# Optimization experiments

Hardware: AMD Instinct MI355X
Metric: run time of the kernel (lower is better)

## Reference

```python
import jax, jax.numpy as jnp
import numpy as np

N, E, D, ED, L = 40000, 640000, 128, 16, 3  # nodes, edges, emb_dim, edge_dim, num_layer
BN_EPS = 1e-5


def setup_inputs() -> dict:
    key = jax.random.key(0)
    ks = jax.random.split(key, 20)
    s = 0.05
    inp = {
        "x": jax.random.normal(ks[0], (N, D), jnp.float32),
        "edge_attr": jax.random.normal(ks[1], (E, ED), jnp.float32),
        # node encoder Linear(input_dim, emb_dim)
        "node_W": jax.random.normal(ks[2], (D, D), jnp.float32) * s,
        "node_b": jnp.zeros((D,), jnp.float32),
        # per-layer params (leading dim L)
        "edge_W": jax.random.normal(ks[3], (L, ED, D), jnp.float32) * s,
        "edge_b": jnp.zeros((L, D), jnp.float32),
        "attn_W": jax.random.normal(ks[4], (L, 2 * D, 1), jnp.float32) * s,
        "attn_b": jnp.zeros((L, 1), jnp.float32),
        "eps": jnp.zeros((L,), jnp.float32),
        "W1": jax.random.normal(ks[5], (L, D, 2 * D), jnp.float32) * s,
        "b1": jnp.zeros((L, 2 * D), jnp.float32),
        "bn1_g": jnp.ones((L, 2 * D), jnp.float32),
        "bn1_b": jnp.zeros((L, 2 * D), jnp.float32),
        "W2": jax.random.normal(ks[6], (L, 2 * D, D), jnp.float32) * s,
        "b2": jnp.zeros((L, D), jnp.float32),
        "bn_g": jnp.ones((L, D), jnp.float32),
        "bn_b": jnp.zeros((L, D), jnp.float32),
        "edge_index": jax.random.randint(ks[7], (2, E), 0, N, jnp.int32),
    }
    return inp


def _bn_eval(h, g, b):
    # BatchNorm1d in eval with running_mean=0, running_var=1
    return g * h * (1.0 / np.sqrt(1.0 + BN_EPS)) + b


def reference(x, edge_attr, node_W, node_b, edge_W, edge_b, attn_W, attn_b,
              eps, W1, b1, bn1_g, bn1_b, W2, b2, bn_g, bn_b, edge_index):
    src, dst = edge_index[0], edge_index[1]
    h = x @ node_W + node_b  # node_encoder, [N, D]
    for l in range(L):
        e = edge_attr @ edge_W[l] + edge_b[l]       # [E, D] edge embedding
        xj = h[src]                                  # [E, D] source gather
        xi = h[dst]                                  # [E, D] target gather
        a = jax.nn.sigmoid(jnp.concatenate([xi, xj], axis=-1) @ attn_W[l] + attn_b[l])  # [E,1]
        msg = jax.nn.relu(xj * a + e)                # fused per-edge message
        agg = jax.ops.segment_sum(msg, dst, num_segments=N)  # scatter-add aggregate
        z = (1.0 + eps[l]) * h + agg
        # GIN mlp: Linear -> BN(eval) -> ReLU -> Linear
        z = _bn_eval(z @ W1[l] + b1[l], bn1_g[l], bn1_b[l])
        z = jax.nn.relu(z)
        z = z @ W2[l] + b2[l]
        # outer BatchNorm(eval); dropout = identity in eval; JK='last', no residual
        z = _bn_eval(z, bn_g[l], bn_b[l])
        if l < L - 1:
            z = jax.nn.relu(z)
        h = z
    return h
```

## Files before the change

### kernel.cpp

```cpp
#include <hip/hip_runtime.h>
#include <math.h>

#define NN 40000
#define EE 640000
#define DD 128
#define EDD 16
#define LL 3
#define TEB 64

__device__ __constant__ float kBnInv = 0.9999950000374997f;

typedef __bf16 bf16x8 __attribute__((ext_vector_type(8)));
typedef float  f32x16 __attribute__((ext_vector_type(16)));
typedef float  f32x4  __attribute__((ext_vector_type(4)));
typedef float  f32x2  __attribute__((ext_vector_type(2)));

__device__ __forceinline__ unsigned pack_bf2(float a, float b) {
    unsigned ua = __float_as_uint(a), ub = __float_as_uint(b);
    ua = (ua + 0x7fffu + ((ua >> 16) & 1u)) >> 16;
    ub = (ub + 0x7fffu + ((ub >> 16) & 1u)) & 0xffff0000u;
    return ua | ub;
}
__device__ __forceinline__ unsigned short bf16r(float x) {
    unsigned u = __float_as_uint(x);
    u = (u + 0x7fffu + ((u >> 16) & 1u)) >> 16;
    return (unsigned short)u;
}

__global__ __launch_bounds__(256) void node_enc_kernel(
    const float* __restrict__ x, const float* __restrict__ W,
    const float* __restrict__ b,
    const float* __restrict__ aW, const float* __restrict__ eps_p,
    float* __restrict__ h, unsigned* __restrict__ hb,
    float* __restrict__ pi, float* __restrict__ pj, float* __restrict__ z)
{
    __shared__ float xs[32][DD];
    const int t = threadIdx.x;
    const long rowbase = (long)blockIdx.x * 32;

    const float4* x4 = (const float4*)(x + rowbase * DD);
    float4* xs4 = (float4*)&xs[0][0];
#pragma unroll
    for (int i = 0; i < 4; i++) xs4[t + i * 256] = x4[t + i * 256];
    __syncthreads();

    const int c  = (t & 31) * 4;
    const int r0 = (t >> 5) * 4;

    float acc[4][4] = {};
    for (int k4 = 0; k4 < DD; k4 += 4) {
        float4 xr[4];
#pragma unroll
        for (int i = 0; i < 4; i++) xr[i] = *(const float4*)&xs[r0 + i][k4];
#pragma unroll
        for (int kk = 0; kk < 4; kk++) {
            const float4 w = *(const float4*)(W + (k4 + kk) * DD + c);
#pragma unroll
            for (int i = 0; i < 4; i++) {
                const float xv = ((const float*)&xr[i])[kk];
                acc[i][0] = fmaf(xv, w.x, acc[i][0]);
                acc[i][1] = fmaf(xv, w.y, acc[i][1]);
                acc[i][2] = fmaf(xv, w.z, acc[i][2]);
                acc[i][3] = fmaf(xv, w.w, acc[i][3]);
            }
        }
    }
    const float4 bv  = *(const float4*)(b + c);
    const float4 awi = *(const float4*)(aW + c);
    const float4 awj = *(const float4*)(aW + DD + c);
    const float ep = 1.0f + eps_p[0];

    float pa[4], pb[4];
#pragma unroll
    for (int i = 0; i < 4; i++) {
        const long row = rowbase + r0 + i;
        float4 ov = { acc[i][0] + bv.x, acc[i][1] + bv.y,
                      acc[i][2] + bv.z, acc[i][3] + bv.w };
        *(float4*)(h + row * DD + c) = ov;
        uint2 pv = { pack_bf2(ov.x, ov.y), pack_bf2(ov.z, ov.w) };
        *(uint2*)(hb + row * 64 + (c >> 1)) = pv;
        float4 zv = { ep * ov.x, ep * ov.y, ep * ov.z, ep * ov.w };
        *(float4*)(z + row * DD + c) = zv;
        pa[i] = ov.x * awi.x + ov.y * awi.y + ov.z * awi.z + ov.w * awi.w;
        pb[i] = ov.x * awj.x + ov.y * awj.y + ov.z * awj.z + ov.w * awj.w;
    }
#pragma unroll
    for (int off = 1; off < 32; off <<= 1) {
#pragma unroll
        for (int i = 0; i < 4; i++) {
            pa[i] += __shfl_xor(pa[i], off, 64);
            pb[i] += __shfl_xor(pb[i], off, 64);
        }
    }
    if ((t & 31) == 0) {
#pragma unroll
        for (int i = 0; i < 4; i++) {
            pi[rowbase + r0 + i] = pa[i];
            pj[rowbase + r0 + i] = pb[i];
        }
    }
}

__global__ __launch_bounds__(256) void wcast_kernel(
    const float* __restrict__ W1, const float* __restrict__ W2,
    const float* __restrict__ eW,
    unsigned short* __restrict__ w1t, unsigned short* __restrict__ w2t,
    unsigned short* __restrict__ ewt)
{
    const int idx = blockIdx.x * 256 + threadIdx.x;
    const int l = idx >> 15, r = idx & 32767;
    {   const int n = r >> 7, k = r & 127;
        w1t[idx] = bf16r(W1[(l << 15) + (k << 8) + n]);
    }
    {   const int n = r >> 8, k = r & 255;
        w2t[idx] = bf16r(W2[(l << 15) + (k << 7) + n]);
    }
    if (idx < LL * 2048) {
        const int le = idx >> 11, re = idx & 2047;
        const int n = re >> 4, k = re & 15;
        ewt[idx] = bf16r(eW[(le << 11) + (k << 7) + n]);
    }
}

__global__ __launch_bounds__(256) void hist_kernel(
    const int* __restrict__ edge_index, int* __restrict__ counts)
{
    const int i = blockIdx.x * 256 + threadIdx.x;
    atomicAdd(&counts[edge_index[EE + i]], 1);
}

__global__ __launch_bounds__(256) void scan1_kernel(
    const int* __restrict__ counts, int* __restrict__ scanned,
    int* __restrict__ partials)
{
    __shared__ int sdata[256];
    const int t = threadIdx.x;
    const int base = blockIdx.x * 1024 + t * 4;
    int v[4]; int sum = 0;
#pragma unroll
    for (int i = 0; i < 4; i++) {
        const int idx = base + i;
        v[i] = (idx < NN) ? counts[idx] : 0;
        sum += v[i];
    }
    sdata[t] = sum;
    __syncthreads();
    for (int off = 1; off < 256; off <<= 1) {
        int x = (t >= off) ? sdata[t - off] : 0;
        __syncthreads();
        sdata[t] += x;
        __syncthreads();
    }
    int run = sdata[t] - sum;
#pragma unroll
    for (int i = 0; i < 4; i++) {
        const int idx = base + i;
        if (idx < NN) scanned[idx] = run;
        run += v[i];
    }
    if (t == 255) partials[blockIdx.x] = sdata[255];
}

__global__ void scan2_kernel(int* __restrict__ partials)
{
    if (threadIdx.x == 0) {
        int run = 0;
        for (int i = 0; i < 40; i++) { int v = partials[i]; partials[i] = run; run += v; }
    }
}

__global__ __launch_bounds__(256) void scan3_kernel(
    const int* __restrict__ scanned, const int* __restrict__ partials,
    int* __restrict__ offsets, int* __restrict__ cursor)
{
    const int idx = blockIdx.x * 256 + threadIdx.x;
    if (idx < NN) {
        const int off = scanned[idx] + partials[idx >> 10];
        offsets[idx] = off;
        cursor[idx]  = off;
    }
}

__global__ __launch_bounds__(256) void scatter_kernel(
    const int* __restrict__ edge_index, const float* __restrict__ edge_attr,
    int* __restrict__ cursor,
    int* __restrict__ srcs_p, int* __restrict__ dstd_p,
    unsigned* __restrict__ ea_b)
{
    const int i = blockIdx.x * 256 + threadIdx.x;
    const int src = edge_index[i];
    const int dst = edge_index[EE + i];
    const int pos = atomicAdd(&cursor[dst], 1);
    srcs_p[pos] = src << 6;
    dstd_p[pos] = dst << 7;

    const float4* sp = (const float4*)(edge_attr + (long)i * EDD);
    const float4 s0 = sp[0], s1 = sp[1], s2 = sp[2], s3 = sp[3];
    uint4 o0 = { pack_bf2(s0.x, s0.y), pack_bf2(s0.z, s0.w),
                 pack_bf2(s1.x, s1.y), pack_bf2(s1.z, s1.w) };
    uint4 o1 = { pack_bf2(s2.x, s2.y), pack_bf2(s2.z, s2.w),
                 pack_bf2(s3.x, s3.y), pack_bf2(s3.z, s3.w) };
    *(uint4*)(ea_b + (long)pos * 8)     = o0;
    *(uint4*)(ea_b + (long)pos * 8 + 4) = o1;
}

__global__ __launch_bounds__(256) void edge_msg_kernel(
    const unsigned* __restrict__ hb, const unsigned* __restrict__ ea_b,
    const float* __restrict__ pi, const float* __restrict__ pj,
    const int* __restrict__ srcs_p, const int* __restrict__ dstd_p,
    const float* __restrict__ ab_p,
    const unsigned short* __restrict__ eWt, const float* __restrict__ eb,
    float* __restrict__ z)
{
    __shared__ float sh_e[TEB * DD];
    __shared__ int   sh_src[TEB];
    __shared__ int   sh_dst[TEB];
    __shared__ float sh_a[TEB];

    const int t = threadIdx.x;
    const int wid = t >> 6, lane = t & 63;
    const long e0 = (long)blockIdx.x * TEB;

    if (t < TEB) {
        const int ss = srcs_p[e0 + t];
        const int dd = dstd_p[e0 + t];
        sh_src[t] = ss;
        sh_dst[t] = dd;
        const float s = pi[dd >> 7] + pj[ss >> 6] + ab_p[0];
        sh_a[t] = 1.0f / (1.0f + expf(-s));
    }

    const int l31 = lane & 31, half = lane >> 5;
    const int mt = wid & 1, nt0 = wid >> 1;
    const bf16x8 afr  = *(const bf16x8*)(ea_b + (e0 + mt * 32 + l31) * 8 + half * 4);
    const bf16x8 bfr0 = *(const bf16x8*)(eWt + (nt0 * 32 + l31) * 16 + half * 8);
    const bf16x8 bfr1 = *(const bf16x8*)(eWt + ((nt0 + 2) * 32 + l31) * 16 + half * 8);

    __syncthreads();

    const int base = wid * 16;
    unsigned u[16];
#pragma unroll
    for (int j = 0; j < 16; j++)
        u[j] = hb[sh_src[base + j] + lane];

    {
        f32x16 a0 = {0.0f,0.0f,0.0f,0.0f, 0.0f,0.0f,0.0f,0.0f,
                     0.0f,0.0f,0.0f,0.0f, 0.0f,0.0f,0.0f,0.0f};
        f32x16 a1 = a0;
        a0 = __builtin_amdgcn_mfma_f32_32x32x16_bf16(afr, bfr0, a0, 0, 0, 0);
        a1 = __builtin_amdgcn_mfma_f32_32x32x16_bf16(afr, bfr1, a1, 0, 0, 0);
        const float eb0 = eb[nt0 * 32 + l31];
        const float eb1 = eb[(nt0 + 2) * 32 + l31];
        const int rb = mt * 32 + 4 * half;
#pragma unroll
        for (int r = 0; r < 16; r++) {
            const int row = rb + (r & 3) + 8 * (r >> 2);
            sh_e[row * DD + nt0 * 32 + l31]       = a0[r] + eb0;
            sh_e[row * DD + (nt0 + 2) * 32 + l31] = a1[r] + eb1;
        }
    }
    __syncthreads();

    const int c0 = lane * 2;
    const f32x2 zero2 = { 0.0f, 0.0f };
    f32x2 acc = zero2;
    int cur = sh_dst[base];

#pragma unroll
    for (int j = 0; j < 16; j++) {
        const int dd = sh_dst[base + j];
        if (dd != cur) {
            atomicAdd(&z[cur + c0],     acc[0]);
            atomicAdd(&z[cur + c0 + 1], acc[1]);
            acc = zero2; cur = dd;
        }
        const float a = sh_a[base + j];
        const f32x2 ev = *(const f32x2*)&sh_e[(base + j) * DD + c0];
        const f32x2 xj = { __uint_as_float(u[j] << 16),
                           __uint_as_float(u[j] & 0xffff0000u) };
        const f32x2 av = { a, a };
        f32x2 m = __builtin_elementwise_fma(xj, av, ev);
        m = __builtin_elementwise_max(m, zero2);
        acc += m;
    }
    atomicAdd(&z[cur + c0],     acc[0]);
    atomicAdd(&z[cur + c0 + 1], acc[1]);
}

__global__ __launch_bounds__(256) void mlp_mfma_kernel(
    const float* __restrict__ zin,
    const unsigned short* __restrict__ w1t, const unsigned short* __restrict__ w2t,
    const float* __restrict__ b1, const float* __restrict__ g1, const float* __restrict__ bb1,
    const float* __restrict__ b2, const float* __restrict__ g2, const float* __restrict__ bb2,
    const float* __restrict__ aWn, const float* __restrict__ epsn_p,
    float* __restrict__ out, unsigned* __restrict__ hb,
    float* __restrict__ pi, float* __restrict__ pj, float* __restrict__ z,
    const int do_relu)
{
    __shared__ __align__(16) unsigned short zsb[64][136];
    __shared__ __align__(16) unsigned short usb[64][264];
    __shared__ float sh_pi[64], sh_pj[64];
    const int t = threadIdx.x;
    const int wid = t >> 6, lane = t & 63;
    const long rowbase = (long)blockIdx.x * 64;

    if (t < 64) { sh_pi[t] = 0.0f; sh_pj[t] = 0.0f; }

    {
        const float4* z4 = (const float4*)(zin + rowbase * DD);
#pragma unroll
        for (int i = 0; i < 8; i++) {
            const int idx = t + i * 256;
            const float4 v = z4[idx];
            const int row = idx >> 5;
            const int c4  = (idx & 31) * 4;
            uint2 pv = { pack_bf2(v.x, v.y), pack_bf2(v.z, v.w) };
            *(uint2*)&zsb[row][c4] = pv;
        }
    }
    __syncthreads();

    const int mrow  = lane & 15;
    const int quad  = lane >> 4;
    const f32x4 vzero = {0.0f, 0.0f, 0.0f, 0.0f};

    {
        const int nt0 = wid * 4;
        bf16x8 bf[4][4];
#pragma unroll
        for (int j = 0; j < 4; j++) {
            const unsigned short* wp = w1t + ((nt0 + j) * 16 + mrow) * 128 + quad * 8;
#pragma unroll
            for (int ks = 0; ks < 4; ks++)
                bf[j][ks] = *(const bf16x8*)(wp + ks * 32);
        }
        float gg[4], bi[4], bt[4];
#pragma unroll
        for (int j = 0; j < 4; j++) {
            const int c = (nt0 + j) * 16 + mrow;
            gg[j] = g1[c]; bi[j] = b1[c]; bt[j] = bb1[c];
        }
#pragma unroll
        for (int rt = 0; rt < 4; rt++) {
            bf16x8 af[4];
#pragma unroll
            for (int ks = 0; ks < 4; ks++)
                af[ks] = *(const bf16x8*)&zsb[rt * 16 + mrow][ks * 32 + quad * 8];
            f32x4 acc[4];
#pragma unroll
            for (int j = 0; j < 4; j++) acc[j] = vzero;
#pragma unroll
            for (int j = 0; j < 4; j++)
#pragma unroll
                for (int ks = 0; ks < 4; ks++)
                    acc[j] = __builtin_amdgcn_mfma_f32_16x16x32_bf16(af[ks], bf[j][ks], acc[j], 0, 0, 0);
#pragma unroll
            for (int j = 0; j < 4; j++) {
                const int c = (nt0 + j) * 16 + mrow;
#pragma unroll
                for (int r = 0; r < 4; r++) {
                    const int row = rt * 16 + quad * 4 + r;
                    const float u = fmaxf(fmaf(gg[j] * (acc[j][r] + bi[j]), kBnInv, bt[j]), 0.0f);
                    const float up = __shfl_xor(u, 1, 64);
                    if ((mrow & 1) == 0)
                        *(unsigned*)&usb[row][c] = pack_bf2(u, up);
                }
            }
        }
    }
    __syncthreads();

    {
        const int nt0 = wid * 2;
        bf16x8 bf[2][8];
#pragma unroll
        for (int j = 0; j < 2; j++) {
            const unsigned short* wp = w2t + ((nt0 + j) * 16 + mrow) * 256 + quad * 8;
#pragma unroll
            for (int ks = 0; ks < 8; ks++)
                bf[j][ks] = *(const bf16x8*)(wp + ks * 32);
        }
        float gg[2], bi[2], bt[2], awi[2], awj[2];
#pragma unroll
        for (int j = 0; j < 2; j++) {
            const int c = (nt0 + j) * 16 + mrow;
            gg[j] = g2[c]; bi[j] = b2[c]; bt[j] = bb2[c];
            awi[j] = aWn[c]; awj[j] = aWn[DD + c];
        }
        const float epn = do_relu ? (1.0f + epsn_p[0]) : 0.0f;

#pragma unroll
        for (int rt = 0; rt < 4; rt++) {
            bf16x8 af[8];
#pragma unroll
            for (int ks = 0; ks < 8; ks++)
                af[ks] = *(const bf16x8*)&usb[rt * 16 + mrow][ks * 32 + quad * 8];
            f32x4 acc[2];
            acc[0] = vzero; acc[1] = vzero;
#pragma unroll
            for (int j = 0; j < 2; j++)
#pragma unroll
                for (int ks = 0; ks < 8; ks++)
                    acc[j] = __builtin_amdgcn_mfma_f32_16x16x32_bf16(af[ks], bf[j][ks], acc[j], 0, 0, 0);

            float si[4] = {0, 0, 0, 0}, sj[4] = {0, 0, 0, 0};
#pragma unroll
            for (int j = 0; j < 2; j++) {
                const int c = (nt0 + j) * 16 + mrow;
#pragma unroll
                for (int r = 0; r < 4; r++) {
                    const long row = rowbase + rt * 16 + quad * 4 + r;
                    float v = fmaf(gg[j] * (acc[j][r] + bi[j]), kBnInv, bt[j]);
                    if (do_relu) {
                        v = fmaxf(v, 0.0f);
                        z[row * DD + c] = epn * v;
                        si[r] = fmaf(v, awi[j], si[r]);
                        sj[r] = fmaf(v, awj[j], sj[r]);
                    }
                    out[row * DD + c] = v;
                    const float vp = __shfl_xor(v, 1, 64);
                    if ((mrow & 1) == 0)
                        hb[row * 64 + (c >> 1)] = pack_bf2(v, vp);
                }
            }
            if (do_relu) {
#pragma unroll
                for (int off = 1; off < 16; off <<= 1) {
#pragma unroll
                    for (int r = 0; r < 4; r++) {
                        si[r] += __shfl_xor(si[r], off, 64);
                        sj[r] += __shfl_xor(sj[r], off, 64);
                    }
                }
                if (mrow == 0) {
#pragma unroll
                    for (int r = 0; r < 4; r++) {
                        atomicAdd(&sh_pi[rt * 16 + quad * 4 + r], si[r]);
                        atomicAdd(&sh_pj[rt * 16 + quad * 4 + r], sj[r]);
                    }
                }
            }
        }
    }
    if (do_relu) {
        __syncthreads();
        if (t < 64) {
            pi[rowbase + t] = sh_pi[t];
            pj[rowbase + t] = sh_pj[t];
        }
    }
}

extern "C" void kernel_launch(void* const* d_in, const int* in_sizes, int n_in,
                              void* d_out, int out_size, void* d_ws, size_t ws_size,
                              hipStream_t stream)
{
    const float* x         = (const float*)d_in[0];
    const float* edge_attr = (const float*)d_in[1];
    const float* node_W    = (const float*)d_in[2];
    const float* node_b    = (const float*)d_in[3];
    const float* edge_W    = (const float*)d_in[4];
    const float* edge_b    = (const float*)d_in[5];
    const float* attn_W    = (const float*)d_in[6];
    const float* attn_b    = (const float*)d_in[7];
    const float* eps       = (const float*)d_in[8];
    const float* W1        = (const float*)d_in[9];
    const float* b1        = (const float*)d_in[10];
    const float* bn1_g     = (const float*)d_in[11];
    const float* bn1_b     = (const float*)d_in[12];
    const float* W2        = (const float*)d_in[13];
    const float* b2        = (const float*)d_in[14];
    const float* bn_g      = (const float*)d_in[15];
    const float* bn_b      = (const float*)d_in[16];
    const int*   edge_index= (const int*)d_in[17];

    float* h    = (float*)d_ws;
    float* z    = h + (size_t)NN * DD;
    float* pi   = z + (size_t)NN * DD;
    float* pj   = pi + NN;
    unsigned* ea_b = (unsigned*)(pj + NN);
    unsigned* hbuf = ea_b + (size_t)EE * 8;
    unsigned short* w1t = (unsigned short*)(hbuf + (size_t)NN * 64);
    unsigned short* w2t = w1t + (size_t)LL * 32768;
    unsigned short* ewt = w2t + (size_t)LL * 32768;
    int* counts  = (int*)(ewt + (size_t)LL * 2048);
    int* offsets = counts + NN;
    int* cursor  = offsets + NN;
    int* scanned = cursor + NN;
    int* partials= scanned + 40960;
    int* srcs_p  = partials + 64;
    int* dstd_p  = srcs_p + EE;
    float* out = (float*)d_out;

    node_enc_kernel<<<NN / 32, 256, 0, stream>>>(
        x, node_W, node_b, attn_W, eps, h, hbuf, pi, pj, z);
    wcast_kernel<<<LL * 128, 256, 0, stream>>>(W1, W2, edge_W, w1t, w2t, ewt);

    hipMemsetAsync(counts, 0, NN * sizeof(int), stream);
    hist_kernel<<<EE / 256, 256, 0, stream>>>(edge_index, counts);
    scan1_kernel<<<40, 256, 0, stream>>>(counts, scanned, partials);
    scan2_kernel<<<1, 64, 0, stream>>>(partials);
    scan3_kernel<<<(NN + 255) / 256, 256, 0, stream>>>(scanned, partials, offsets, cursor);
    scatter_kernel<<<EE / 256, 256, 0, stream>>>(
        edge_index, edge_attr, cursor, srcs_p, dstd_p, ea_b);

    for (int l = 0; l < LL; l++) {
        const int ln = (l + 1 < LL) ? (l + 1) : l;
        edge_msg_kernel<<<EE / TEB, 256, 0, stream>>>(
            hbuf, ea_b, pi, pj, srcs_p, dstd_p, attn_b + l,
            ewt + (size_t)l * 2048, edge_b + (size_t)l * DD, z);
        mlp_mfma_kernel<<<NN / 64, 256, 0, stream>>>(
            z,
            w1t + (size_t)l * 32768, w2t + (size_t)l * 32768,
            b1 + (size_t)l * 2 * DD, bn1_g + (size_t)l * 2 * DD, bn1_b + (size_t)l * 2 * DD,
            b2 + (size_t)l * DD, bn_g + (size_t)l * DD, bn_b + (size_t)l * DD,
            attn_W + (size_t)ln * 2 * DD, eps + ln,
            (l == LL - 1) ? out : h, hbuf, pi, pj, z, (l < LL - 1) ? 1 : 0);
    }
}
```

Before: 533.1 us.

## Assign destination-node ranges per wave in edge kernel, replacing atomics with plain stores

The edge message kernel now gives each wavefront a contiguous range of 4 destination nodes, found through the CSR offsets. Because no other wave writes those nodes, the atomic scatter-adds into z become plain read-modify-write float2 stores. Each wave computes its own edge embeddings with MFMA into a per-wave bf16 LDS tile. Source, destination and attention values are shared with wave shuffles instead of block-level syncs. The costs are load imbalance from varying node degree, bf16 rounding of the edge embedding, and partial 32-edge chunks at range boundaries.

Result: slower. 831.8 us (+56.0%).

```diff
diff --git a/kernel.cpp b/kernel.cpp
--- a/kernel.cpp
+++ b/kernel.cpp
@@ -6,7 +6,7 @@
 #define DD 128
 #define EDD 16
 #define LL 3
-#define TEB 64
+#define KPW 4
 
 __device__ __constant__ float kBnInv = 0.9999950000374997f;
 
@@ -208,84 +208,102 @@
     const unsigned* __restrict__ hb, const unsigned* __restrict__ ea_b,
     const float* __restrict__ pi, const float* __restrict__ pj,
     const int* __restrict__ srcs_p, const int* __restrict__ dstd_p,
-    const float* __restrict__ ab_p,
+    const int* __restrict__ offsets, const float* __restrict__ ab_p,
     const unsigned short* __restrict__ eWt, const float* __restrict__ eb,
     float* __restrict__ z)
 {
-    __shared__ float sh_e[TEB * DD];
-    __shared__ int   sh_src[TEB];
-    __shared__ int   sh_dst[TEB];
-    __shared__ float sh_a[TEB];
+    __shared__ __align__(16) unsigned short et[4][32 * DD];
 
     const int t = threadIdx.x;
     const int wid = t >> 6, lane = t & 63;
-    const long e0 = (long)blockIdx.x * TEB;
-
-    if (t < TEB) {
-        const int ss = srcs_p[e0 + t];
-        const int dd = dstd_p[e0 + t];
-        sh_src[t] = ss;
-        sh_dst[t] = dd;
-        const float s = pi[dd >> 7] + pj[ss >> 6] + ab_p[0];
-        sh_a[t] = 1.0f / (1.0f + expf(-s));
-    }
+    const int n0 = (blockIdx.x * 4 + wid) * KPW;
+    const int ebeg = offsets[n0];
+    const int eend = (n0 + KPW < NN) ? offsets[n0 + KPW] : EE;
 
     const int l31 = lane & 31, half = lane >> 5;
-    const int mt = wid & 1, nt0 = wid >> 1;
-    const bf16x8 afr  = *(const bf16x8*)(ea_b + (e0 + mt * 32 + l31) * 8 + half * 4);
-    const bf16x8 bfr0 = *(const bf16x8*)(eWt + (nt0 * 32 + l31) * 16 + half * 8);
-    const bf16x8 bfr1 = *(const bf16x8*)(eWt + ((nt0 + 2) * 32 + l31) * 16 + half * 8);
-
-    __syncthreads();
-
-    const int base = wid * 16;
-    unsigned u[16];
-#pragma unroll
-    for (int j = 0; j < 16; j++)
-        u[j] = hb[sh_src[base + j] + lane];
-
-    {
-        f32x16 a0 = {0.0f,0.0f,0.0f,0.0f, 0.0f,0.0f,0.0f,0.0f,
-                     0.0f,0.0f,0.0f,0.0f, 0.0f,0.0f,0.0f,0.0f};
-        f32x16 a1 = a0;
-        a0 = __builtin_amdgcn_mfma_f32_32x32x16_bf16(afr, bfr0, a0, 0, 0, 0);
-        a1 = __builtin_amdgcn_mfma_f32_32x32x16_bf16(afr, bfr1, a1, 0, 0, 0);
-        const float eb0 = eb[nt0 * 32 + l31];
-        const float eb1 = eb[(nt0 + 2) * 32 + l31];
-        const int rb = mt * 32 + 4 * half;
-#pragma unroll
-        for (int r = 0; r < 16; r++) {
-            const int row = rb + (r & 3) + 8 * (r >> 2);
-            sh_e[row * DD + nt0 * 32 + l31]       = a0[r] + eb0;
-            sh_e[row * DD + (nt0 + 2) * 32 + l31] = a1[r] + eb1;
-        }
-    }
-    __syncthreads();
-
+    bf16x8 bfr[4];
+#pragma unroll
+    for (int nt = 0; nt < 4; nt++)
+        bfr[nt] = *(const bf16x8*)(eWt + (nt * 32 + l31) * 16 + half * 8);
+    float ebv[4];
+#pragma unroll
+    for (int nt = 0; nt < 4; nt++) ebv[nt] = eb[nt * 32 + l31];
+    const float ab0 = ab_p[0];
+    const int rb = 4 * half;
+    unsigned short* etw = et[wid];
     const int c0 = lane * 2;
     const f32x2 zero2 = { 0.0f, 0.0f };
+    const f32x16 vz16 = {0.0f,0.0f,0.0f,0.0f, 0.0f,0.0f,0.0f,0.0f,
+                         0.0f,0.0f,0.0f,0.0f, 0.0f,0.0f,0.0f,0.0f};
+
     f32x2 acc = zero2;
-    int cur = sh_dst[base];
-
-#pragma unroll
-    for (int j = 0; j < 16; j++) {
-        const int dd = sh_dst[base + j];
-        if (dd != cur) {
-            atomicAdd(&z[cur + c0],     acc[0]);
-            atomicAdd(&z[cur + c0 + 1], acc[1]);
-            acc = zero2; cur = dd;
-        }
-        const float a = sh_a[base + j];
-        const f32x2 ev = *(const f32x2*)&sh_e[(base + j) * DD + c0];
-        const f32x2 xj = { __uint_as_float(u[j] << 16),
-                           __uint_as_float(u[j] & 0xffff0000u) };
-        const f32x2 av = { a, a };
-        f32x2 m = __builtin_elementwise_fma(xj, av, ev);
-        m = __builtin_elementwise_max(m, zero2);
-        acc += m;
-    }
-    atomicAdd(&z[cur + c0],     acc[0]);
-    atomicAdd(&z[cur + c0 + 1], acc[1]);
+    int cur = -1;
+
+    for (int e = ebeg; e < eend; e += 32) {
+        const int rem = eend - e;
+        const int nv = rem < 32 ? rem : 32;
+
+        const int ce = min(e + l31, EE - 1);
+        const int ss = srcs_p[ce];
+        const int dd = dstd_p[ce];
+        const float s  = pi[dd >> 7] + pj[ss >> 6] + ab0;
+        const float av = 1.0f / (1.0f + expf(-s));
+
+        unsigned u0[16], u1[16];
+#pragma unroll
+        for (int j = 0; j < 16; j++)
+            if (j < nv) u0[j] = hb[__shfl(ss, j, 64) + lane];
+#pragma unroll
+        for (int j = 0; j < 16; j++)
+            if (16 + j < nv) u1[j] = hb[__shfl(ss, 16 + j, 64) + lane];
+
+        const bf16x8 afr = *(const bf16x8*)(ea_b + (long)ce * 8 + half * 4);
+#pragma unroll
+        for (int p = 0; p < 2; p++) {
+            f32x16 a0 = vz16, a1 = vz16;
+            a0 = __builtin_amdgcn_mfma_f32_32x32x16_bf16(afr, bfr[2 * p],     a0, 0, 0, 0);
+            a1 = __builtin_amdgcn_mfma_f32_32x32x16_bf16(afr, bfr[2 * p + 1], a1, 0, 0, 0);
+#pragma unroll
+            for (int r = 0; r < 16; r++) {
+                const int row = rb + (r & 3) + 8 * (r >> 2);
+                etw[row * DD + (2 * p)     * 32 + l31] = bf16r(a0[r] + ebv[2 * p]);
+                etw[row * DD + (2 * p + 1) * 32 + l31] = bf16r(a1[r] + ebv[2 * p + 1]);
+            }
+        }
+        asm volatile("" ::: "memory");
+
+#pragma unroll
+        for (int j = 0; j < 32; j++) {
+            if (j >= nv) break;
+            const int ddj = __shfl(dd, j, 64);
+            if (ddj != cur) {
+                if (cur >= 0) {
+                    float2 zv = *(const float2*)(z + cur + c0);
+                    zv.x += acc[0]; zv.y += acc[1];
+                    *(float2*)(z + cur + c0) = zv;
+                }
+                acc = zero2; cur = ddj;
+            }
+            const float aj = __shfl(av, j, 64);
+            const unsigned uj = (j < 16) ? u0[j & 15] : u1[j & 15];
+            const unsigned el = (unsigned)etw[j * DD + c0];
+            const unsigned eh = (unsigned)etw[j * DD + c0 + 1];
+            const f32x2 ev = { __uint_as_float(el << 16),
+                               __uint_as_float(eh << 16) };
+            const f32x2 xj = { __uint_as_float(uj << 16),
+                               __uint_as_float(uj & 0xffff0000u) };
+            const f32x2 avv = { aj, aj };
+            f32x2 m = __builtin_elementwise_fma(xj, avv, ev);
+            m = __builtin_elementwise_max(m, zero2);
+            acc += m;
+        }
+        asm volatile("" ::: "memory");
+    }
+    if (cur >= 0) {
+        float2 zv = *(const float2*)(z + cur + c0);
+        zv.x += acc[0]; zv.y += acc[1];
+        *(float2*)(z + cur + c0) = zv;
+    }
 }
 
 __global__ __launch_bounds__(256) void mlp_mfma_kernel(
@@ -507,8 +525,8 @@
 
     for (int l = 0; l < LL; l++) {
         const int ln = (l + 1 < LL) ? (l + 1) : l;
-        edge_msg_kernel<<<EE / TEB, 256, 0, stream>>>(
-            hbuf, ea_b, pi, pj, srcs_p, dstd_p, attn_b + l,
+        edge_msg_kernel<<<NN / (4 * KPW), 256, 0, stream>>>(
+            hbuf, ea_b, pi, pj, srcs_p, dstd_p, offsets, attn_b + l,
             ewt + (size_t)l * 2048, edge_b + (size_t)l * DD, z);
         mlp_mfma_kernel<<<NN / 64, 256, 0, stream>>>(
             z,
```
